# Kernel tuning notes

Hardware: AMD Instinct MI355X
Metric: run time of the kernel (lower is better)

Reference implementation:

```python
import jax, jax.numpy as jnp
import numpy as np

EPS = 1e-06
M = 10.0
IGNORE_LABEL = 100  # setup guarantees no label == 100, so the torch filter is a no-op


def setup_inputs() -> dict:
    key = jax.random.key(0)
    kf, kl = jax.random.split(key)
    n, d = 8192, 128
    features = jax.random.normal(kf, (n, d), dtype=jnp.float32)
    labels = jax.random.randint(kl, (n,), 0, 16, dtype=jnp.int64)
    return {"features": features, "labels": labels}


def reference(features, labels):
    # features: (n, d) float; labels: (n,) int, none equal to IGNORE_LABEL
    n = features.shape[0]
    dt = features.dtype

    # pairwise squared euclidean distances via Gram trick (avoids (n,n,d) tensor)
    sq = jnp.sum(features * features, axis=1)              # (n,)
    ed = sq[:, None] + sq[None, :] - 2.0 * (features @ features.T)  # (n, n)

    eq = labels[:, None] == labels[None, :]                # (n, n), includes diagonal
    counts = jnp.sum(eq, axis=1, keepdims=True).astype(dt) - 1.0  # (n, 1)

    eqf = eq.astype(dt)
    w = eqf / (counts + EPS) - (1.0 - eqf) / (n - counts - 1.0 + EPS)
    w = w * (1.0 - jnp.eye(n, dtype=dt))                   # zero diagonal

    loss = jnp.sum(w * ed, axis=1) + M                     # (n,)
    valid = (counts[:, 0] != 0.0).astype(dt)               # rows with same-class neighbors
    return jnp.sum(jax.nn.relu(loss) * valid) / jnp.maximum(jnp.sum(valid), 1.0)
```

## Files before the change

### kernel.cpp

```cpp
#include <hip/hip_runtime.h>

#define NCLASS 16
#define D 128
#define EPSF 1e-6f
#define MF 10.0f

#define WS_PART 16
#define SLOT 2080

#define AGG_BLOCKS 64
#define AGG_THREADS 512
#define AGG_WAVES 8

__global__ void __launch_bounds__(AGG_THREADS)
agg_kernel(const float* __restrict__ F, const int* __restrict__ L,
           float* __restrict__ ws, int n) {
    __shared__ __align__(16) float Ssh[AGG_WAVES][NCLASS * D];
    __shared__ float qsh[AGG_WAVES][NCLASS];
    __shared__ float csh[AGG_WAVES][NCLASS];
    const int tid  = threadIdx.x;
    const int lane = tid & 63;
    const int wv   = tid >> 6;
    const int sub  = lane & 31;
    const int half = lane >> 5;
    const int gw   = blockIdx.x * AGG_WAVES + wv;
    const int nwv  = AGG_BLOCKS * AGG_WAVES;
    const int npairs = n >> 1;

    float sx[NCLASS], sy[NCLASS], sz[NCLASS], sw[NCLASS], qa[NCLASS], ca[NCLASS];
    #pragma unroll
    for (int c = 0; c < NCLASS; ++c) { sx[c]=sy[c]=sz[c]=sw[c]=qa[c]=ca[c]=0.f; }

    const float4* __restrict__ F4 = (const float4*)F;
    for (int rp = gw; rp < npairs; rp += nwv) {
        const int r = rp * 2 + half;
        const int lc = L[r];
        const float4 v = F4[(size_t)r * 32 + sub];
        const float vv = fmaf(v.x, v.x, fmaf(v.y, v.y, fmaf(v.z, v.z, v.w*v.w)));
        #pragma unroll
        for (int c = 0; c < NCLASS; ++c) {
            const float sel = (lc == c) ? 1.f : 0.f;
            sx[c] = fmaf(sel, v.x, sx[c]);
            sy[c] = fmaf(sel, v.y, sy[c]);
            sz[c] = fmaf(sel, v.z, sz[c]);
            sw[c] = fmaf(sel, v.w, sw[c]);
            qa[c] = fmaf(sel, vv,  qa[c]);
            ca[c] += sel;
        }
    }
    #pragma unroll
    for (int c = 0; c < NCLASS; ++c) {
        sx[c] += __shfl_xor(sx[c], 32, 64);
        sy[c] += __shfl_xor(sy[c], 32, 64);
        sz[c] += __shfl_xor(sz[c], 32, 64);
        sw[c] += __shfl_xor(sw[c], 32, 64);
        float q = qa[c], cc = ca[c];
        #pragma unroll
        for (int off = 32; off; off >>= 1) {
            q  += __shfl_xor(q, off, 64);
            cc += __shfl_xor(cc, off, 64);
        }
        qa[c] = q; ca[c] = cc;
    }
    if (half == 0) {
        #pragma unroll
        for (int c = 0; c < NCLASS; ++c)
            ((float4*)&Ssh[wv][c * D])[sub] = make_float4(sx[c], sy[c], sz[c], sw[c]);
    }
    if (lane == 0) {
        #pragma unroll
        for (int c = 0; c < NCLASS; ++c) {
            qsh[wv][c] = qa[c];
            csh[wv][c] = ca[c] * (1.f / 32.f);
        }
    }
    __syncthreads();
    float* __restrict__ base = ws + WS_PART + (size_t)blockIdx.x * SLOT;
    {
        float4 a = make_float4(0.f, 0.f, 0.f, 0.f);
        #pragma unroll
        for (int w = 0; w < AGG_WAVES; ++w) {
            const float4 t = ((const float4*)Ssh[w])[tid];
            a.x += t.x; a.y += t.y; a.z += t.z; a.w += t.w;
        }
        ((float4*)base)[tid] = a;
    }
    if (tid < NCLASS) {
        float q = 0.f, cc = 0.f;
        #pragma unroll
        for (int w = 0; w < AGG_WAVES; ++w) { q += qsh[w][tid]; cc += csh[w][tid]; }
        base[NCLASS * D + tid] = q;
        base[NCLASS * D + NCLASS + tid] = cc;
    }
    if (blockIdx.x == 0 && tid == 0) {
        ws[0] = 0.f; ws[1] = 0.f;
        ((unsigned*)ws)[2] = 0u;
    }
}

#define LOSS_BLOCKS 256
#define LOSS_THREADS 256
#define LOSS_WAVES 4

__global__ void __launch_bounds__(LOSS_THREADS)
loss_kernel(const float* __restrict__ F, float* __restrict__ ws,
            const int* __restrict__ L, float* __restrict__ out, int n) {
    __shared__ __align__(16) float S_lds[NCLASS * D];
    __shared__ float Stot[D];
    __shared__ float Q_lds[NCLASS];
    __shared__ float cnt_lds[NCLASS];
    __shared__ float Qtot_s;
    __shared__ float redL[LOSS_WAVES], redV[LOSS_WAVES];

    const int tid = threadIdx.x;
    const float* __restrict__ pb = ws + WS_PART;
    for (int p = tid; p < NCLASS * D / 4; p += LOSS_THREADS) {
        float4 a = make_float4(0.f, 0.f, 0.f, 0.f);
        for (int s = 0; s < AGG_BLOCKS; ++s) {
            const float4 t = ((const float4*)(pb + (size_t)s * SLOT))[p];
            a.x += t.x; a.y += t.y; a.z += t.z; a.w += t.w;
        }
        ((float4*)S_lds)[p] = a;
    }
    if (tid < NCLASS) {
        float q = 0.f, cc = 0.f;
        for (int s = 0; s < AGG_BLOCKS; ++s) {
            q  += pb[(size_t)s * SLOT + NCLASS * D + tid];
            cc += pb[(size_t)s * SLOT + NCLASS * D + NCLASS + tid];
        }
        Q_lds[tid] = q; cnt_lds[tid] = cc;
    }
    __syncthreads();
    if (tid < D) {
        float s = 0.f;
        #pragma unroll
        for (int c = 0; c < NCLASS; ++c) s += S_lds[c * D + tid];
        Stot[tid] = s;
    }
    if (tid == 0) {
        float q = 0.f;
        #pragma unroll
        for (int c = 0; c < NCLASS; ++c) q += Q_lds[c];
        Qtot_s = q;
    }
    __syncthreads();

    const int lane = tid & 63;
    const int wv = tid >> 6;
    const int gw = blockIdx.x * LOSS_WAVES + wv;
    const int nw = LOSS_BLOCKS * LOSS_WAVES;
    const float nf = (float)n;
    const float2* __restrict__ F2 = (const float2*)F;
    const float2* __restrict__ S2 = (const float2*)S_lds;
    const float2* __restrict__ T2 = (const float2*)Stot;

    float accL = 0.f, accV = 0.f;
    #pragma unroll 2
    for (int r = gw; r < n; r += nw) {
        const int c = L[r];
        const float2 v = F2[(size_t)r * 64 + lane];
        const float2 a = S2[c * 64 + lane];
        const float2 t = T2[lane];
        float sq    = fmaf(v.x, v.x, v.y * v.y);
        float dsame = fmaf(v.x, a.x, v.y * a.y);
        float dtot  = fmaf(v.x, t.x, v.y * t.y);
        #pragma unroll
        for (int off = 32; off; off >>= 1) {
            sq    += __shfl_xor(sq, off, 64);
            dsame += __shfl_xor(dsame, off, 64);
            dtot  += __shfl_xor(dtot, off, 64);
        }
        const float cntc   = cnt_lds[c];
        const float counts = cntc - 1.f;
        const float same_sum = counts * sq + sq + Q_lds[c] - 2.f * dsame;
        const float diff_sum = (nf - cntc) * sq + (Qtot_s - Q_lds[c])
                               - 2.f * (dtot - dsame);
        const float loss = same_sum / (counts + EPSF)
                         - diff_sum / (nf - cntc + EPSF) + MF;
        const float valid = counts > 0.5f ? 1.f : 0.f;
        accL += (loss > 0.f ? loss : 0.f) * valid;
        accV += valid;
    }
    if (lane == 0) { redL[wv] = accL; redV[wv] = accV; }
    __syncthreads();
    if (tid == 0) {
        float sL = 0.f, sV = 0.f;
        #pragma unroll
        for (int w = 0; w < LOSS_WAVES; ++w) { sL += redL[w]; sV += redV[w]; }
        atomicAdd(&ws[0], sL);
        atomicAdd(&ws[1], sV);
        __threadfence();
        unsigned done = __hip_atomic_fetch_add((unsigned*)ws + 2, 1u,
                                               __ATOMIC_ACQ_REL,
                                               __HIP_MEMORY_SCOPE_AGENT);
        if (done == (unsigned)(LOSS_BLOCKS - 1)) {
            float sl = __hip_atomic_load(&ws[0], __ATOMIC_RELAXED,
                                         __HIP_MEMORY_SCOPE_AGENT);
            float sv = __hip_atomic_load(&ws[1], __ATOMIC_RELAXED,
                                         __HIP_MEMORY_SCOPE_AGENT);
            out[0] = sl / fmaxf(sv, 1.f);
        }
    }
}

extern "C" void kernel_launch(void* const* d_in, const int* in_sizes, int n_in,
                              void* d_out, int out_size, void* d_ws, size_t ws_size,
                              hipStream_t stream) {
    const float* F = (const float*)d_in[0];
    const int* L = (const int*)d_in[1];
    float* out = (float*)d_out;
    float* ws = (float*)d_ws;
    const int n = in_sizes[1];

    agg_kernel<<<AGG_BLOCKS, AGG_THREADS, 0, stream>>>(F, L, ws, n);
    loss_kernel<<<LOSS_BLOCKS, LOSS_THREADS, 0, stream>>>(F, ws, L, out, n);
}
```

Baseline: 91.12 us.

## Reduce aggregation partials once via grid barrier instead of per loss block

The aggregation kernel now publishes per-block partials, spins on per-block flags as a grid barrier, then cooperatively reduces the 64 partial slots into a single final array. Loss blocks copy that final array instead of each re-summing all 64 slots. The final loss reduction replaces float atomics with per-block partial writes plus a last-block tree reduction. The flags are never cleared between launches, so later calls may pass the barrier early and read stale partials, and the barrier relies on all aggregation blocks being co-resident.

```diff
diff --git a/kernel.cpp b/kernel.cpp
--- a/kernel.cpp
+++ b/kernel.cpp
@@ -5,12 +5,31 @@
 #define EPSF 1e-6f
 #define MF 10.0f
 
-#define WS_PART 16
-#define SLOT 2080
-
 #define AGG_BLOCKS 64
 #define AGG_THREADS 512
 #define AGG_WAVES 8
+#define LOSS_BLOCKS 256
+#define LOSS_THREADS 256
+#define LOSS_WAVES 4
+
+#define WS_CTR   0
+#define WS_FA    16
+#define WS_FLAGS 2112
+#define WS_PART  2176
+#define SLOT     2080
+#define WS_LP    (WS_PART + AGG_BLOCKS * SLOT)
+#define MAGIC    0xBEEF1234u
+
+__device__ __forceinline__ float4 wave_sum_f4(float4 v) {
+    #pragma unroll
+    for (int off = 32; off; off >>= 1) {
+        v.x += __shfl_xor(v.x, off, 64);
+        v.y += __shfl_xor(v.y, off, 64);
+        v.z += __shfl_xor(v.z, off, 64);
+        v.w += __shfl_xor(v.w, off, 64);
+    }
+    return v;
+}
 
 __global__ void __launch_bounds__(AGG_THREADS)
 agg_kernel(const float* __restrict__ F, const int* __restrict__ L,
@@ -27,6 +46,8 @@
     const int nwv  = AGG_BLOCKS * AGG_WAVES;
     const int npairs = n >> 1;
 
+    if (blockIdx.x == 0 && tid == 0) ((unsigned*)ws)[WS_CTR] = 0u;
+
     float sx[NCLASS], sy[NCLASS], sz[NCLASS], sw[NCLASS], qa[NCLASS], ca[NCLASS];
     #pragma unroll
     for (int c = 0; c < NCLASS; ++c) { sx[c]=sy[c]=sz[c]=sw[c]=qa[c]=ca[c]=0.f; }
@@ -92,15 +113,34 @@
         base[NCLASS * D + tid] = q;
         base[NCLASS * D + NCLASS + tid] = cc;
     }
-    if (blockIdx.x == 0 && tid == 0) {
-        ws[0] = 0.f; ws[1] = 0.f;
-        ((unsigned*)ws)[2] = 0u;
-    }
-}
-
-#define LOSS_BLOCKS 256
-#define LOSS_THREADS 256
-#define LOSS_WAVES 4
+    __syncthreads();
+    if (tid == 0) {
+        __threadfence();
+        __hip_atomic_store((unsigned*)(ws + WS_FLAGS) + blockIdx.x, MAGIC,
+                           __ATOMIC_RELEASE, __HIP_MEMORY_SCOPE_AGENT);
+    }
+    if (tid < AGG_BLOCKS) {
+        const unsigned* fl = (const unsigned*)(ws + WS_FLAGS) + tid;
+        while (__hip_atomic_load(fl, __ATOMIC_ACQUIRE,
+                                 __HIP_MEMORY_SCOPE_AGENT) != MAGIC) {
+            __builtin_amdgcn_s_sleep(2);
+        }
+    }
+    __syncthreads();
+    __threadfence();
+    const float4* __restrict__ P4 = (const float4*)(ws + WS_PART);
+    float4* __restrict__ FA4 = (float4*)(ws + WS_FA);
+    {
+        const int p = blockIdx.x * AGG_WAVES + wv;
+        float4 v = wave_sum_f4(P4[(size_t)lane * (SLOT / 4) + p]);
+        if (lane == 0) FA4[p] = v;
+    }
+    if (blockIdx.x < (SLOT / 4 - 512) && wv == 0) {
+        const int p2 = 512 + blockIdx.x;
+        float4 v = wave_sum_f4(P4[(size_t)lane * (SLOT / 4) + p2]);
+        if (lane == 0) FA4[p2] = v;
+    }
+}
 
 __global__ void __launch_bounds__(LOSS_THREADS)
 loss_kernel(const float* __restrict__ F, float* __restrict__ ws,
@@ -111,24 +151,15 @@
     __shared__ float cnt_lds[NCLASS];
     __shared__ float Qtot_s;
     __shared__ float redL[LOSS_WAVES], redV[LOSS_WAVES];
+    __shared__ int isLast;
 
     const int tid = threadIdx.x;
-    const float* __restrict__ pb = ws + WS_PART;
-    for (int p = tid; p < NCLASS * D / 4; p += LOSS_THREADS) {
-        float4 a = make_float4(0.f, 0.f, 0.f, 0.f);
-        for (int s = 0; s < AGG_BLOCKS; ++s) {
-            const float4 t = ((const float4*)(pb + (size_t)s * SLOT))[p];
-            a.x += t.x; a.y += t.y; a.z += t.z; a.w += t.w;
-        }
-        ((float4*)S_lds)[p] = a;
-    }
+    const float4* __restrict__ FA4 = (const float4*)(ws + WS_FA);
+    for (int p = tid; p < NCLASS * D / 4; p += LOSS_THREADS)
+        ((float4*)S_lds)[p] = FA4[p];
     if (tid < NCLASS) {
-        float q = 0.f, cc = 0.f;
-        for (int s = 0; s < AGG_BLOCKS; ++s) {
-            q  += pb[(size_t)s * SLOT + NCLASS * D + tid];
-            cc += pb[(size_t)s * SLOT + NCLASS * D + NCLASS + tid];
-        }
-        Q_lds[tid] = q; cnt_lds[tid] = cc;
+        Q_lds[tid]   = ws[WS_FA + NCLASS * D + tid];
+        cnt_lds[tid] = ws[WS_FA + NCLASS * D + NCLASS + tid];
     }
     __syncthreads();
     if (tid < D) {
@@ -187,17 +218,29 @@
         float sL = 0.f, sV = 0.f;
         #pragma unroll
         for (int w = 0; w < LOSS_WAVES; ++w) { sL += redL[w]; sV += redV[w]; }
-        atomicAdd(&ws[0], sL);
-        atomicAdd(&ws[1], sV);
+        ((float2*)(ws + WS_LP))[blockIdx.x] = make_float2(sL, sV);
         __threadfence();
-        unsigned done = __hip_atomic_fetch_add((unsigned*)ws + 2, 1u,
-                                               __ATOMIC_ACQ_REL,
-                                               __HIP_MEMORY_SCOPE_AGENT);
-        if (done == (unsigned)(LOSS_BLOCKS - 1)) {
-            float sl = __hip_atomic_load(&ws[0], __ATOMIC_RELAXED,
-                                         __HIP_MEMORY_SCOPE_AGENT);
-            float sv = __hip_atomic_load(&ws[1], __ATOMIC_RELAXED,
-                                         __HIP_MEMORY_SCOPE_AGENT);
+        unsigned old = __hip_atomic_fetch_add((unsigned*)ws + WS_CTR, 1u,
+                                              __ATOMIC_ACQ_REL,
+                                              __HIP_MEMORY_SCOPE_AGENT);
+        isLast = (old == (unsigned)(LOSS_BLOCKS - 1)) ? 1 : 0;
+    }
+    __syncthreads();
+    if (isLast) {
+        __threadfence();
+        const float2 pr = ((const float2*)(ws + WS_LP))[tid];
+        float l = pr.x, v = pr.y;
+        #pragma unroll
+        for (int off = 32; off; off >>= 1) {
+            l += __shfl_xor(l, off, 64);
+            v += __shfl_xor(v, off, 64);
+        }
+        if (lane == 0) { redL[wv] = l; redV[wv] = v; }
+        __syncthreads();
+        if (tid == 0) {
+            float sl = 0.f, sv = 0.f;
+            #pragma unroll
+            for (int w = 0; w < LOSS_WAVES; ++w) { sl += redL[w]; sv += redV[w]; }
             out[0] = sl / fmaxf(sv, 1.f);
         }
     }
```

New measurement: 95.45 us. +4.8%, slower.
